# Optimization experiments

Measured on AMD Instinct MI355X. Metric: run time of the kernel, lower is better.

## Reference

```python
import jax, jax.numpy as jnp
import numpy as np

N_NODES = 50000
N_EDGES = 800000
D = 128


def gcn_conv(x, W, b, src, dst, num_nodes):
    """PyG GCNConv: x @ W, add self-loops, symmetric normalization, scatter-add, + bias."""
    x = x @ W  # [N, out]
    loop = jnp.arange(num_nodes, dtype=src.dtype)
    s = jnp.concatenate([src, loop])  # [E+N]
    d = jnp.concatenate([dst, loop])
    w = jnp.ones(s.shape[0], x.dtype)  # edge_weight=None -> ones (self-loop fill=1)
    deg = jax.ops.segment_sum(w, d, num_segments=num_nodes)  # [N]
    dinv = jnp.where(deg > 0, jax.lax.rsqrt(deg), 0.0)
    norm = dinv[s] * dinv[d]  # [E+N]
    out = jax.ops.segment_sum(x[s] * norm[:, None], d, num_segments=num_nodes)
    return out + b


def setup_inputs() -> dict:
    key = jax.random.key(0)
    ks = jax.random.split(key, 8)
    sc = 1.0 / np.sqrt(D)
    x = jax.random.normal(ks[0], (N_NODES, D), dtype=jnp.float32)
    edge_index = jax.random.randint(ks[1], (2, N_EDGES), 0, N_NODES)
    W1 = jax.random.normal(ks[2], (D, D), dtype=jnp.float32) * sc
    W2 = jax.random.normal(ks[3], (D, D), dtype=jnp.float32) * sc
    W3 = jax.random.normal(ks[4], (D, D), dtype=jnp.float32) * sc
    b1 = jnp.zeros((D,), jnp.float32)
    b2 = jnp.zeros((D,), jnp.float32)
    b3 = jnp.zeros((D,), jnp.float32)
    return {"x": x, "edge_index": edge_index, "W1": W1, "b1": b1,
            "W2": W2, "b2": b2, "W3": W3, "b3": b3}


def reference(x, edge_index, W1, b1, W2, b2, W3, b3):
    src, dst = edge_index[0], edge_index[1]
    n = x.shape[0]
    x = jax.nn.relu(gcn_conv(x, W1, b1, src, dst, n))
    x = jax.nn.relu(gcn_conv(x, W2, b2, src, dst, n))
    return gcn_conv(x, W3, b3, src, dst, n)
```

## Files before the change

kernel.cpp:

```cpp
#include <hip/hip_runtime.h>
#include <hip/hip_fp16.h>
#include <math.h>

#define D 128
#define PADH 136

typedef __attribute__((ext_vector_type(8))) _Float16 half8;
typedef __attribute__((ext_vector_type(4))) _Float16 half4v;
typedef __attribute__((ext_vector_type(4))) float f32x4;


__global__ void prep_kernel(const float* __restrict__ W1, const float* __restrict__ W2,
                            const float* __restrict__ W3, __half* __restrict__ WhT,
                            int* __restrict__ cnt, int N) {
    int i = blockIdx.x * blockDim.x + threadIdx.x;
    if (i < 3 * D * D) {
        int l = i >> 14;
        int j = i & 16383;
        int n = j >> 7, k = j & 127;
        const float* W = (l == 0) ? W1 : (l == 1) ? W2 : W3;
        WhT[(size_t)i] = __float2half(W[(size_t)k * D + n]);
    }
    if (i < N) cnt[i] = 0;
}


__global__ void count_rank_kernel(const int* __restrict__ dst, int* __restrict__ cnt,
                                  int* __restrict__ rank, int E) {
    int e0 = (blockIdx.x * blockDim.x + threadIdx.x) * 8;
    if (e0 + 7 < E) {
        int4 da = *(const int4*)(dst + e0);
        int4 db = *(const int4*)(dst + e0 + 4);
        int4 ra, rb;
        ra.x = atomicAdd(&cnt[da.x], 1);
        ra.y = atomicAdd(&cnt[da.y], 1);
        ra.z = atomicAdd(&cnt[da.z], 1);
        ra.w = atomicAdd(&cnt[da.w], 1);
        rb.x = atomicAdd(&cnt[db.x], 1);
        rb.y = atomicAdd(&cnt[db.y], 1);
        rb.z = atomicAdd(&cnt[db.z], 1);
        rb.w = atomicAdd(&cnt[db.w], 1);
        *(int4*)(rank + e0)     = ra;
        *(int4*)(rank + e0 + 4) = rb;
    } else {
        for (int e = e0; e < E; ++e) rank[e] = atomicAdd(&cnt[dst[e]], 1);
    }
}

__global__ __launch_bounds__(1024) void scan_kernel(const int* __restrict__ cnt,
                                                    int* __restrict__ rowptr,
                                                    float* __restrict__ dinv,
                                                    int N) {
    __shared__ int wsum[16];
    int tid  = threadIdx.x;
    int lane = tid & 63;
    int wid  = tid >> 6;
    int C = ((N + 4095) / 4096) * 4;
    int start = tid * C;
    int end   = start + C; if (end > N) end = N;

    int local = 0;
    int i = start;
    for (; i + 3 < end; i += 4) {
        int4 v = *(const int4*)(cnt + i);
        local += v.x + v.y + v.z + v.w;
    }
    for (; i < end; ++i) local += cnt[i];

    int sc = local;
    #pragma unroll
    for (int off = 1; off < 64; off <<= 1) {
        int t = __shfl_up(sc, off, 64);
        if (lane >= off) sc += t;
    }
    if (lane == 63) wsum[wid] = sc;
    __syncthreads();
    if (tid < 16) {
        int w = wsum[tid];
        #pragma unroll
        for (int off = 1; off < 16; off <<= 1) {
            int t = __shfl_up(w, off, 16);
            if (tid >= off) w += t;
        }
        wsum[tid] = w;
    }
    __syncthreads();
    int run = ((wid > 0) ? wsum[wid - 1] : 0) + (sc - local);

    i = start;
    for (; i + 3 < end; i += 4) {
        int4 v = *(const int4*)(cnt + i);
        int4 rp;
        rp.x = run;
        rp.y = rp.x + v.x;
        rp.z = rp.y + v.y;
        rp.w = rp.z + v.z;
        run  = rp.w + v.w;
        *(int4*)(rowptr + i) = rp;
        float4 dv;
        dv.x = rsqrtf((float)v.x + 1.0f);
        dv.y = rsqrtf((float)v.y + 1.0f);
        dv.z = rsqrtf((float)v.z + 1.0f);
        dv.w = rsqrtf((float)v.w + 1.0f);
        *(float4*)(dinv + i) = dv;
    }
    for (; i < end; ++i) {
        int v = cnt[i];
        rowptr[i] = run; run += v;
        dinv[i] = rsqrtf((float)v + 1.0f);
    }
    if (tid == 0) rowptr[N] = wsum[15];
}


__device__ __forceinline__ float4 gather2(const __half* __restrict__ g,
                                          const int* __restrict__ rowptr,
                                          const int* __restrict__ col,
                                          int r0, int r1, int lane) {
    int half = lane >> 5;
    int l32  = lane & 31;
    int hb   = half << 5;
    int row  = half ? r1 : r0;
    int s = rowptr[row], e = rowptr[row + 1];

    half4v hs = ((const half4v*)(g + (size_t)row * D))[l32];
    float4 A = make_float4((float)hs[0], (float)hs[1], (float)hs[2], (float)hs[3]);
    float4 B = make_float4(0.f, 0.f, 0.f, 0.f);

    for (int base = s; base < e; base += 32) {
        int idx = base + l32;
        int myc = (idx < e) ? col[idx] : 0;
        int nb  = min(32, e - base);
        int j = 0;
        for (; j + 8 <= nb; j += 8) {
            int c0 = __shfl(myc, hb + j + 0), c1 = __shfl(myc, hb + j + 1);
            int c2 = __shfl(myc, hb + j + 2), c3 = __shfl(myc, hb + j + 3);
            int c4 = __shfl(myc, hb + j + 4), c5 = __shfl(myc, hb + j + 5);
            int c6 = __shfl(myc, hb + j + 6), c7 = __shfl(myc, hb + j + 7);
            half4v v0 = ((const half4v*)(g + (size_t)c0 * D))[l32];
            half4v v1 = ((const half4v*)(g + (size_t)c1 * D))[l32];
            half4v v2 = ((const half4v*)(g + (size_t)c2 * D))[l32];
            half4v v3 = ((const half4v*)(g + (size_t)c3 * D))[l32];
            half4v v4 = ((const half4v*)(g + (size_t)c4 * D))[l32];
            half4v v5 = ((const half4v*)(g + (size_t)c5 * D))[l32];
            half4v v6 = ((const half4v*)(g + (size_t)c6 * D))[l32];
            half4v v7 = ((const half4v*)(g + (size_t)c7 * D))[l32];
            A.x += (float)v0[0]; A.y += (float)v0[1]; A.z += (float)v0[2]; A.w += (float)v0[3];
            B.x += (float)v1[0]; B.y += (float)v1[1]; B.z += (float)v1[2]; B.w += (float)v1[3];
            A.x += (float)v2[0]; A.y += (float)v2[1]; A.z += (float)v2[2]; A.w += (float)v2[3];
            B.x += (float)v3[0]; B.y += (float)v3[1]; B.z += (float)v3[2]; B.w += (float)v3[3];
            A.x += (float)v4[0]; A.y += (float)v4[1]; A.z += (float)v4[2]; A.w += (float)v4[3];
            B.x += (float)v5[0]; B.y += (float)v5[1]; B.z += (float)v5[2]; B.w += (float)v5[3];
            A.x += (float)v6[0]; A.y += (float)v6[1]; A.z += (float)v6[2]; A.w += (float)v6[3];
            B.x += (float)v7[0]; B.y += (float)v7[1]; B.z += (float)v7[2]; B.w += (float)v7[3];
        }
        for (; j + 4 <= nb; j += 4) {
            int c0 = __shfl(myc, hb + j + 0), c1 = __shfl(myc, hb + j + 1);
            int c2 = __shfl(myc, hb + j + 2), c3 = __shfl(myc, hb + j + 3);
            half4v v0 = ((const half4v*)(g + (size_t)c0 * D))[l32];
            half4v v1 = ((const half4v*)(g + (size_t)c1 * D))[l32];
            half4v v2 = ((const half4v*)(g + (size_t)c2 * D))[l32];
            half4v v3 = ((const half4v*)(g + (size_t)c3 * D))[l32];
            A.x += (float)v0[0]; A.y += (float)v0[1]; A.z += (float)v0[2]; A.w += (float)v0[3];
            B.x += (float)v1[0]; B.y += (float)v1[1]; B.z += (float)v1[2]; B.w += (float)v1[3];
            A.x += (float)v2[0]; A.y += (float)v2[1]; A.z += (float)v2[2]; A.w += (float)v2[3];
            B.x += (float)v3[0]; B.y += (float)v3[1]; B.z += (float)v3[2]; B.w += (float)v3[3];
        }
        for (; j < nb; ++j) {
            int c = __shfl(myc, hb + j);
            half4v v = ((const half4v*)(g + (size_t)c * D))[l32];
            A.x += (float)v[0]; A.y += (float)v[1]; A.z += (float)v[2]; A.w += (float)v[3];
        }
    }
    A.x += B.x; A.y += B.y; A.z += B.z; A.w += B.w;
    return A;
}


__global__ __launch_bounds__(256) void fill_gemm1_kernel(
    const int* __restrict__ src, const int* __restrict__ dst,
    const int* __restrict__ rank, const int* __restrict__ rowptr,
    int* __restrict__ col, int E, int fill_blocks,
    const float* __restrict__ X, const __half* __restrict__ WhT,
    const float* __restrict__ dinv, __half* __restrict__ Y, int M) {
    int tid = threadIdx.x;
    if ((int)blockIdx.x < fill_blocks) {
        int e0 = (blockIdx.x * 256 + tid) * 8;
        if (e0 + 7 < E) {
            int4 da = *(const int4*)(dst + e0);
            int4 db = *(const int4*)(dst + e0 + 4);
            int4 ra = *(const int4*)(rank + e0);
            int4 rb = *(const int4*)(rank + e0 + 4);
            int4 sa = *(const int4*)(src + e0);
            int4 sb = *(const int4*)(src + e0 + 4);
            int p0 = rowptr[da.x] + ra.x;
            int p1 = rowptr[da.y] + ra.y;
            int p2 = rowptr[da.z] + ra.z;
            int p3 = rowptr[da.w] + ra.w;
            int p4 = rowptr[db.x] + rb.x;
            int p5 = rowptr[db.y] + rb.y;
            int p6 = rowptr[db.z] + rb.z;
            int p7 = rowptr[db.w] + rb.w;
            col[p0] = sa.x; col[p1] = sa.y; col[p2] = sa.z; col[p3] = sa.w;
            col[p4] = sb.x; col[p5] = sb.y; col[p6] = sb.z; col[p7] = sb.w;
        } else {
            for (int e = e0; e < E; ++e) col[rowptr[dst[e]] + rank[e]] = src[e];
        }
        return;
    }
    int bid  = blockIdx.x - fill_blocks;
    int wave = tid >> 6;
    int lane = tid & 63;
    int quad = lane >> 4;
    int l16  = lane & 15;
    int m0   = bid * 64 + wave * 16;
    if (m0 >= M) return;

    f32x4 acc[8];
    #pragma unroll
    for (int t = 0; t < 8; ++t) acc[t] = (f32x4)0.0f;

    const float* xrow = X + (size_t)(m0 + l16) * D;

    #pragma unroll
    for (int ks = 0; ks < 4; ++ks) {
        int k0 = ks * 32 + quad * 8;
        float4 x0 = *(const float4*)(xrow + k0);
        float4 x1 = *(const float4*)(xrow + k0 + 4);
        half8 a;
        a[0] = (_Float16)x0.x; a[1] = (_Float16)x0.y;
        a[2] = (_Float16)x0.z; a[3] = (_Float16)x0.w;
        a[4] = (_Float16)x1.x; a[5] = (_Float16)x1.y;
        a[6] = (_Float16)x1.z; a[7] = (_Float16)x1.w;
        #pragma unroll
        for (int t = 0; t < 8; ++t) {
            half8 b = *(const half8*)(WhT + (size_t)(t * 16 + l16) * D + k0);
            acc[t] = __builtin_amdgcn_mfma_f32_16x16x32_f16(a, b, acc[t], 0, 0, 0);
        }
    }

    float4 dv = *(const float4*)(dinv + m0 + quad * 4);
    float dvs[4] = {dv.x, dv.y, dv.z, dv.w};
    #pragma unroll
    for (int t = 0; t < 8; ++t) {
        #pragma unroll
        for (int r = 0; r < 4; ++r) {
            int grow = m0 + quad * 4 + r;
            Y[(size_t)grow * D + t * 16 + l16] = __float2half(acc[t][r] * dvs[r]);
        }
    }
}


__global__ __launch_bounds__(256) void agg_gemm_kernel(
    const __half* __restrict__ ysIn, const int* __restrict__ rowptr,
    const int* __restrict__ col, const float* __restrict__ dinv,
    const float* __restrict__ bias, const __half* __restrict__ WhT,
    __half* __restrict__ ysOut, int M) {
    __shared__ __half lds_h[16 * PADH];
    int tid  = threadIdx.x;
    int wave = tid >> 6;
    int lane = tid & 63;
    int half = lane >> 5;
    int l32  = lane & 31;
    int rbase = blockIdx.x * 16;

    float4 bb = ((const float4*)bias)[l32];
    #pragma unroll
    for (int t = 0; t < 2; ++t) {
        int lr0 = wave * 4 + t * 2;
        int row0 = rbase + lr0;
        int row1 = row0 + 1;
        int c0 = min(row0, M - 1);
        int c1 = min(row1, M - 1);
        float4 a = gather2(ysIn, rowptr, col, c0, c1, lane);
        int myrow = half ? c1 : c0;
        float dv = dinv[myrow];
        half4v hv;
        hv[0] = (_Float16)fmaxf(bb.x + dv * a.x, 0.f);
        hv[1] = (_Float16)fmaxf(bb.y + dv * a.y, 0.f);
        hv[2] = (_Float16)fmaxf(bb.z + dv * a.z, 0.f);
        hv[3] = (_Float16)fmaxf(bb.w + dv * a.w, 0.f);
        ((half4v*)(lds_h + (size_t)(lr0 + half) * PADH))[l32] = hv;
    }
    __syncthreads();

    if (rbase >= M) return;
    int quad = lane >> 4;
    int l16  = lane & 15;
    int t0   = wave * 2;

    f32x4 acc0 = (f32x4)0.0f, acc1 = (f32x4)0.0f;
    const __half* arow = lds_h + (size_t)l16 * PADH;

    #pragma unroll
    for (int ks = 0; ks < 4; ++ks) {
        int k0 = ks * 32 + quad * 8;
        half8 a  = *(const half8*)(arow + k0);
        half8 b0 = *(const half8*)(WhT + (size_t)((t0 + 0) * 16 + l16) * D + k0);
        half8 b1 = *(const half8*)(WhT + (size_t)((t0 + 1) * 16 + l16) * D + k0);
        acc0 = __builtin_amdgcn_mfma_f32_16x16x32_f16(a, b0, acc0, 0, 0, 0);
        acc1 = __builtin_amdgcn_mfma_f32_16x16x32_f16(a, b1, acc1, 0, 0, 0);
    }

    #pragma unroll
    for (int r = 0; r < 4; ++r) {
        int grow = rbase + quad * 4 + r;
        if (grow < M) {
            float dvr = dinv[grow];
            ysOut[(size_t)grow * D + (t0 + 0) * 16 + l16] = __float2half(acc0[r] * dvr);
            ysOut[(size_t)grow * D + (t0 + 1) * 16 + l16] = __float2half(acc1[r] * dvr);
        }
    }
}


__global__ __launch_bounds__(256) void agg_final_kernel(
    const __half* __restrict__ ys, const int* __restrict__ rowptr,
    const int* __restrict__ col, const float* __restrict__ dinv,
    const float* __restrict__ b, float* __restrict__ out, int N) {
    int gwave = (blockIdx.x * blockDim.x + threadIdx.x) >> 6;
    int lane  = threadIdx.x & 63;
    int half  = lane >> 5;
    int l32   = lane & 31;
    int row0  = gwave * 2;
    if (row0 >= N) return;
    int row1  = row0 + 1;
    int c1    = min(row1, N - 1);

    float4 a = gather2(ys, rowptr, col, row0, c1, lane);
    int myrow = half ? c1 : row0;
    int orow  = row0 + half;
    if (orow < N) {
        float dv  = dinv[myrow];
        float4 bb = ((const float4*)b)[l32];
        float4 r;
        r.x = bb.x + dv * a.x;
        r.y = bb.y + dv * a.y;
        r.z = bb.z + dv * a.z;
        r.w = bb.w + dv * a.w;
        ((float4*)(out + (size_t)orow * D))[l32] = r;
    }
}


extern "C" void kernel_launch(void* const* d_in, const int* in_sizes, int n_in,
                              void* d_out, int out_size, void* d_ws, size_t ws_size,
                              hipStream_t stream) {
    const float* x   = (const float*)d_in[0];
    const int*   ei  = (const int*)d_in[1];
    const float* W1  = (const float*)d_in[2];
    const float* b1  = (const float*)d_in[3];
    const float* W2  = (const float*)d_in[4];
    const float* b2  = (const float*)d_in[5];
    const float* W3  = (const float*)d_in[6];
    const float* b3  = (const float*)d_in[7];
    float* out = (float*)d_out;

    const int N = in_sizes[0] / D;
    const int E = in_sizes[1] / 2;
    const int* src = ei;
    const int* dst = ei + E;

    char* ws = (char*)d_ws;
    size_t off = 0;
    auto alloc = [&](size_t bytes) {
        void* p = ws + off;
        off = (off + bytes + 255) & ~(size_t)255;
        return p;
    };
    __half* ys    = (__half*)alloc((size_t)N * D * sizeof(__half));
    __half* hs    = (__half*)alloc((size_t)N * D * sizeof(__half));
    int*   cnt    = (int*)alloc((size_t)N * sizeof(int));
    int*   rowptr = (int*)alloc((size_t)(N + 1) * sizeof(int));
    float* dinv   = (float*)alloc((size_t)N * sizeof(float));
    int*   rank   = (int*)alloc((size_t)E * sizeof(int));
    int*   col    = (int*)alloc((size_t)E * sizeof(int));
    __half* WhT   = (__half*)alloc((size_t)3 * D * D * sizeof(__half));
    (void)ws_size; (void)n_in; (void)out_size;

    int prep_threads = (3 * D * D > N) ? 3 * D * D : N;
    prep_kernel<<<(prep_threads + 255) / 256, 256, 0, stream>>>(W1, W2, W3, WhT, cnt, N);

    const int egrid = ((E + 7) / 8 + 255) / 256;
    count_rank_kernel<<<egrid, 256, 0, stream>>>(dst, cnt, rank, E);
    scan_kernel<<<1, 1024, 0, stream>>>(cnt, rowptr, dinv, N);

    const int gemm1_grid = (N + 63) / 64;
    fill_gemm1_kernel<<<egrid + gemm1_grid, 256, 0, stream>>>(
        src, dst, rank, rowptr, col, E, egrid, x, WhT, dinv, ys, N);

    const int agg_gemm_grid = (N + 15) / 16;
    agg_gemm_kernel<<<agg_gemm_grid, 256, 0, stream>>>(ys, rowptr, col, dinv, b1, WhT + 16384, hs, N);
    agg_gemm_kernel<<<agg_gemm_grid, 256, 0, stream>>>(hs, rowptr, col, dinv, b2, WhT + 32768, ys, N);

    const int aggf_grid = ((N + 1) / 2 * 64 + 255) / 256;
    agg_final_kernel<<<aggf_grid, 256, 0, stream>>>(ys, rowptr, col, dinv, b3, out, N);
}
```

Baseline: 294.2 us.

## Fuse all GCN stages into one cooperative persistent kernel with grid syncs

Replaces the seven-kernel launch sequence with a single cooperative mega-kernel of 1024 blocks that runs every stage (weight transpose, degree count, scan, CSR fill plus first GEMM, two agg+GEMM layers, final aggregation) separated by grid.sync. The single-block scan is replaced by a multi-block scan using per-block partials, and each block serially sums the partials of all earlier blocks. The aim is to remove launch gaps and the serial one-block scan. In exchange, the persistent grid may have lower per-stage occupancy and grid barriers add cost. If the cooperative launch fails, the code falls back to the old kernels.

```diff
diff --git a/kernel.cpp b/kernel.cpp
--- a/kernel.cpp
+++ b/kernel.cpp
@@ -1,116 +1,18 @@
 #include <hip/hip_runtime.h>
 #include <hip/hip_fp16.h>
+#include <hip/hip_cooperative_groups.h>
 #include <math.h>
 
 #define D 128
 #define PADH 136
+#define NB 1024
+#define NT 256
+
+namespace cg = cooperative_groups;
 
 typedef __attribute__((ext_vector_type(8))) _Float16 half8;
 typedef __attribute__((ext_vector_type(4))) _Float16 half4v;
 typedef __attribute__((ext_vector_type(4))) float f32x4;
-
-
-__global__ void prep_kernel(const float* __restrict__ W1, const float* __restrict__ W2,
-                            const float* __restrict__ W3, __half* __restrict__ WhT,
-                            int* __restrict__ cnt, int N) {
-    int i = blockIdx.x * blockDim.x + threadIdx.x;
-    if (i < 3 * D * D) {
-        int l = i >> 14;
-        int j = i & 16383;
-        int n = j >> 7, k = j & 127;
-        const float* W = (l == 0) ? W1 : (l == 1) ? W2 : W3;
-        WhT[(size_t)i] = __float2half(W[(size_t)k * D + n]);
-    }
-    if (i < N) cnt[i] = 0;
-}
-
-
-__global__ void count_rank_kernel(const int* __restrict__ dst, int* __restrict__ cnt,
-                                  int* __restrict__ rank, int E) {
-    int e0 = (blockIdx.x * blockDim.x + threadIdx.x) * 8;
-    if (e0 + 7 < E) {
-        int4 da = *(const int4*)(dst + e0);
-        int4 db = *(const int4*)(dst + e0 + 4);
-        int4 ra, rb;
-        ra.x = atomicAdd(&cnt[da.x], 1);
-        ra.y = atomicAdd(&cnt[da.y], 1);
-        ra.z = atomicAdd(&cnt[da.z], 1);
-        ra.w = atomicAdd(&cnt[da.w], 1);
-        rb.x = atomicAdd(&cnt[db.x], 1);
-        rb.y = atomicAdd(&cnt[db.y], 1);
-        rb.z = atomicAdd(&cnt[db.z], 1);
-        rb.w = atomicAdd(&cnt[db.w], 1);
-        *(int4*)(rank + e0)     = ra;
-        *(int4*)(rank + e0 + 4) = rb;
-    } else {
-        for (int e = e0; e < E; ++e) rank[e] = atomicAdd(&cnt[dst[e]], 1);
-    }
-}
-
-__global__ __launch_bounds__(1024) void scan_kernel(const int* __restrict__ cnt,
-                                                    int* __restrict__ rowptr,
-                                                    float* __restrict__ dinv,
-                                                    int N) {
-    __shared__ int wsum[16];
-    int tid  = threadIdx.x;
-    int lane = tid & 63;
-    int wid  = tid >> 6;
-    int C = ((N + 4095) / 4096) * 4;
-    int start = tid * C;
-    int end   = start + C; if (end > N) end = N;
-
-    int local = 0;
-    int i = start;
-    for (; i + 3 < end; i += 4) {
-        int4 v = *(const int4*)(cnt + i);
-        local += v.x + v.y + v.z + v.w;
-    }
-    for (; i < end; ++i) local += cnt[i];
-
-    int sc = local;
-    #pragma unroll
-    for (int off = 1; off < 64; off <<= 1) {
-        int t = __shfl_up(sc, off, 64);
-        if (lane >= off) sc += t;
-    }
-    if (lane == 63) wsum[wid] = sc;
-    __syncthreads();
-    if (tid < 16) {
-        int w = wsum[tid];
-        #pragma unroll
-        for (int off = 1; off < 16; off <<= 1) {
-            int t = __shfl_up(w, off, 16);
-            if (tid >= off) w += t;
-        }
-        wsum[tid] = w;
-    }
-    __syncthreads();
-    int run = ((wid > 0) ? wsum[wid - 1] : 0) + (sc - local);
-
-    i = start;
-    for (; i + 3 < end; i += 4) {
-        int4 v = *(const int4*)(cnt + i);
-        int4 rp;
-        rp.x = run;
-        rp.y = rp.x + v.x;
-        rp.z = rp.y + v.y;
-        rp.w = rp.z + v.z;
-        run  = rp.w + v.w;
-        *(int4*)(rowptr + i) = rp;
-        float4 dv;
-        dv.x = rsqrtf((float)v.x + 1.0f);
-        dv.y = rsqrtf((float)v.y + 1.0f);
-        dv.z = rsqrtf((float)v.z + 1.0f);
-        dv.w = rsqrtf((float)v.w + 1.0f);
-        *(float4*)(dinv + i) = dv;
-    }
-    for (; i < end; ++i) {
-        int v = cnt[i];
-        rowptr[i] = run; run += v;
-        dinv[i] = rsqrtf((float)v + 1.0f);
-    }
-    if (tid == 0) rowptr[N] = wsum[15];
-}
 
 
 __device__ __forceinline__ float4 gather2(const __half* __restrict__ g,
@@ -177,6 +79,359 @@
 }
 
 
+__global__ __launch_bounds__(NT, 4) void mega_kernel(
+    const float* __restrict__ X, const int* __restrict__ src, const int* __restrict__ dst,
+    const float* __restrict__ W1, const float* __restrict__ b1,
+    const float* __restrict__ W2, const float* __restrict__ b2,
+    const float* __restrict__ W3, const float* __restrict__ b3,
+    float* __restrict__ out,
+    __half* __restrict__ ys, __half* __restrict__ hs,
+    int* __restrict__ cnt, int* __restrict__ rowptr, float* __restrict__ dinv,
+    int* __restrict__ rank, int* __restrict__ col, int* __restrict__ partials,
+    __half* __restrict__ WhT, int N, int E)
+{
+    cg::grid_group grid = cg::this_grid();
+    const int tid  = threadIdx.x;
+    const int bid  = blockIdx.x;
+    const int nb   = gridDim.x;
+    const int gid  = bid * NT + tid;
+    const int gsz  = nb * NT;
+    const int lane = tid & 63;
+    const int wid  = tid >> 6;
+
+    __shared__ __half lds_h[16 * PADH];
+    __shared__ int sred[4];
+
+    for (int i = gid; i < 3 * D * D; i += gsz) {
+        int l = i >> 14, j = i & 16383, n = j >> 7, k = j & 127;
+        const float* W = (l == 0) ? W1 : (l == 1) ? W2 : W3;
+        WhT[i] = __float2half(W[(size_t)k * D + n]);
+    }
+    for (int i = gid; i < N; i += gsz) cnt[i] = 0;
+    grid.sync();
+
+    const int NO = (E + 7) / 8;
+    for (int c = gid; c < NO; c += gsz) {
+        int e0 = c * 8;
+        if (e0 + 7 < E) {
+            int4 da = *(const int4*)(dst + e0);
+            int4 db = *(const int4*)(dst + e0 + 4);
+            int4 ra, rb;
+            ra.x = atomicAdd(&cnt[da.x], 1);
+            ra.y = atomicAdd(&cnt[da.y], 1);
+            ra.z = atomicAdd(&cnt[da.z], 1);
+            ra.w = atomicAdd(&cnt[da.w], 1);
+            rb.x = atomicAdd(&cnt[db.x], 1);
+            rb.y = atomicAdd(&cnt[db.y], 1);
+            rb.z = atomicAdd(&cnt[db.z], 1);
+            rb.w = atomicAdd(&cnt[db.w], 1);
+            *(int4*)(rank + e0)     = ra;
+            *(int4*)(rank + e0 + 4) = rb;
+        } else {
+            for (int e = e0; e < E; ++e) rank[e] = atomicAdd(&cnt[dst[e]], 1);
+        }
+    }
+    grid.sync();
+
+    int4 myv = make_int4(0, 0, 0, 0);
+    int mysum = 0;
+    const int t4 = gid * 4;
+    if (t4 < N) {
+        if (t4 + 3 < N) myv = *(const int4*)(cnt + t4);
+        else {
+            myv.x = cnt[t4];
+            if (t4 + 1 < N) myv.y = cnt[t4 + 1];
+            if (t4 + 2 < N) myv.z = cnt[t4 + 2];
+        }
+        mysum = myv.x + myv.y + myv.z + myv.w;
+        dinv[t4] = rsqrtf((float)myv.x + 1.0f);
+        if (t4 + 1 < N) dinv[t4 + 1] = rsqrtf((float)myv.y + 1.0f);
+        if (t4 + 2 < N) dinv[t4 + 2] = rsqrtf((float)myv.z + 1.0f);
+        if (t4 + 3 < N) dinv[t4 + 3] = rsqrtf((float)myv.w + 1.0f);
+    }
+    {
+        int rs = mysum;
+        #pragma unroll
+        for (int off = 32; off > 0; off >>= 1) rs += __shfl_down(rs, off, 64);
+        if (lane == 0) sred[wid] = rs;
+        __syncthreads();
+        if (tid == 0) partials[bid] = sred[0] + sred[1] + sred[2] + sred[3];
+    }
+    grid.sync();
+
+    {
+        int sc = mysum;
+        #pragma unroll
+        for (int off = 1; off < 64; off <<= 1) {
+            int t = __shfl_up(sc, off, 64);
+            if (lane >= off) sc += t;
+        }
+        __syncthreads();
+        if (lane == 63) sred[wid] = sc;
+        __syncthreads();
+        int waveoff = 0;
+        #pragma unroll
+        for (int w = 0; w < 4; ++w) if (w < wid) waveoff += sred[w];
+        if (t4 < N) {
+            int base = 0;
+            for (int b = 0; b < bid; ++b) base += partials[b];
+            int run = base + waveoff + (sc - mysum);
+            rowptr[t4] = run;                 run += myv.x;
+            if (t4 + 1 < N) rowptr[t4 + 1] = run; run += myv.y;
+            if (t4 + 2 < N) rowptr[t4 + 2] = run; run += myv.z;
+            if (t4 + 3 < N) rowptr[t4 + 3] = run;
+        }
+        if (gid == 0) rowptr[N] = E;
+    }
+    grid.sync();
+
+    const int FB = nb / 2;
+    if (bid < FB) {
+        const int fsz = FB * NT;
+        for (int c = bid * NT + tid; c < NO; c += fsz) {
+            int e0 = c * 8;
+            if (e0 + 7 < E) {
+                int4 da = *(const int4*)(dst + e0);
+                int4 db = *(const int4*)(dst + e0 + 4);
+                int4 ra = *(const int4*)(rank + e0);
+                int4 rb = *(const int4*)(rank + e0 + 4);
+                int4 sa = *(const int4*)(src + e0);
+                int4 sb = *(const int4*)(src + e0 + 4);
+                col[rowptr[da.x] + ra.x] = sa.x;
+                col[rowptr[da.y] + ra.y] = sa.y;
+                col[rowptr[da.z] + ra.z] = sa.z;
+                col[rowptr[da.w] + ra.w] = sa.w;
+                col[rowptr[db.x] + rb.x] = sb.x;
+                col[rowptr[db.y] + rb.y] = sb.y;
+                col[rowptr[db.z] + rb.z] = sb.z;
+                col[rowptr[db.w] + rb.w] = sb.w;
+            } else {
+                for (int e = e0; e < E; ++e) col[rowptr[dst[e]] + rank[e]] = src[e];
+            }
+        }
+    } else {
+        const int ntile = (N + 63) / 64;
+        const int quad = lane >> 4, l16 = lane & 15;
+        for (int t = bid - FB; t < ntile; t += nb - FB) {
+            int m0 = t * 64 + wid * 16;
+            if (m0 < N) {
+                f32x4 acc[8];
+                #pragma unroll
+                for (int q = 0; q < 8; ++q) acc[q] = (f32x4)0.0f;
+                const float* xrow = X + (size_t)(m0 + l16) * D;
+                #pragma unroll
+                for (int ks = 0; ks < 4; ++ks) {
+                    int k0 = ks * 32 + quad * 8;
+                    float4 x0 = *(const float4*)(xrow + k0);
+                    float4 x1 = *(const float4*)(xrow + k0 + 4);
+                    half8 a;
+                    a[0] = (_Float16)x0.x; a[1] = (_Float16)x0.y;
+                    a[2] = (_Float16)x0.z; a[3] = (_Float16)x0.w;
+                    a[4] = (_Float16)x1.x; a[5] = (_Float16)x1.y;
+                    a[6] = (_Float16)x1.z; a[7] = (_Float16)x1.w;
+                    #pragma unroll
+                    for (int q = 0; q < 8; ++q) {
+                        half8 b = *(const half8*)(WhT + (size_t)(q * 16 + l16) * D + k0);
+                        acc[q] = __builtin_amdgcn_mfma_f32_16x16x32_f16(a, b, acc[q], 0, 0, 0);
+                    }
+                }
+                float4 dv = *(const float4*)(dinv + m0 + quad * 4);
+                float dvs[4] = {dv.x, dv.y, dv.z, dv.w};
+                #pragma unroll
+                for (int q = 0; q < 8; ++q) {
+                    #pragma unroll
+                    for (int r = 0; r < 4; ++r) {
+                        int grow = m0 + quad * 4 + r;
+                        ys[(size_t)grow * D + q * 16 + l16] = __float2half(acc[q][r] * dvs[r]);
+                    }
+                }
+            }
+        }
+    }
+    grid.sync();
+
+    #pragma unroll 1
+    for (int layer = 0; layer < 2; ++layer) {
+        const __half* gin   = (layer == 0) ? ys : hs;
+        __half*       gout  = (layer == 0) ? hs : ys;
+        const float*  bias  = (layer == 0) ? b1 : b2;
+        const __half* WhTl  = WhT + (layer == 0 ? 16384 : 32768);
+
+        const int hf  = lane >> 5;
+        const int l32 = lane & 31;
+        const int quad = lane >> 4, l16 = lane & 15;
+        const int t0 = wid * 2;
+        float4 bb = ((const float4*)bias)[l32];
+        const int ntile = (N + 15) / 16;
+
+        for (int tile = bid; tile < ntile; tile += nb) {
+            int rbase = tile * 16;
+            #pragma unroll
+            for (int t = 0; t < 2; ++t) {
+                int lr0 = wid * 4 + t * 2;
+                int row0 = rbase + lr0;
+                int c0 = min(row0, N - 1);
+                int c1 = min(row0 + 1, N - 1);
+                float4 a = gather2(gin, rowptr, col, c0, c1, lane);
+                int myrow = hf ? c1 : c0;
+                float dv = dinv[myrow];
+                half4v hv;
+                hv[0] = (_Float16)fmaxf(bb.x + dv * a.x, 0.f);
+                hv[1] = (_Float16)fmaxf(bb.y + dv * a.y, 0.f);
+                hv[2] = (_Float16)fmaxf(bb.z + dv * a.z, 0.f);
+                hv[3] = (_Float16)fmaxf(bb.w + dv * a.w, 0.f);
+                ((half4v*)(lds_h + (size_t)(lr0 + hf) * PADH))[l32] = hv;
+            }
+            __syncthreads();
+
+            f32x4 acc0 = (f32x4)0.0f, acc1 = (f32x4)0.0f;
+            const __half* arow = lds_h + (size_t)l16 * PADH;
+            #pragma unroll
+            for (int ks = 0; ks < 4; ++ks) {
+                int k0 = ks * 32 + quad * 8;
+                half8 a  = *(const half8*)(arow + k0);
+                half8 b0 = *(const half8*)(WhTl + (size_t)((t0 + 0) * 16 + l16) * D + k0);
+                half8 b1v = *(const half8*)(WhTl + (size_t)((t0 + 1) * 16 + l16) * D + k0);
+                acc0 = __builtin_amdgcn_mfma_f32_16x16x32_f16(a, b0, acc0, 0, 0, 0);
+                acc1 = __builtin_amdgcn_mfma_f32_16x16x32_f16(a, b1v, acc1, 0, 0, 0);
+            }
+            #pragma unroll
+            for (int r = 0; r < 4; ++r) {
+                int grow = rbase + quad * 4 + r;
+                if (grow < N) {
+                    float dvr = dinv[grow];
+                    gout[(size_t)grow * D + (t0 + 0) * 16 + l16] = __float2half(acc0[r] * dvr);
+                    gout[(size_t)grow * D + (t0 + 1) * 16 + l16] = __float2half(acc1[r] * dvr);
+                }
+            }
+            __syncthreads();
+        }
+        grid.sync();
+    }
+
+    {
+        const int gw = gid >> 6;
+        const int nw = gsz >> 6;
+        const int hf = lane >> 5;
+        const int l32 = lane & 31;
+        const int npair = (N + 1) / 2;
+        for (int p = gw; p < npair; p += nw) {
+            int row0 = p * 2;
+            int c1 = min(row0 + 1, N - 1);
+            float4 a = gather2(ys, rowptr, col, row0, c1, lane);
+            int myrow = hf ? c1 : row0;
+            int orow = row0 + hf;
+            if (orow < N) {
+                float dv  = dinv[myrow];
+                float4 bb = ((const float4*)b3)[l32];
+                float4 r;
+                r.x = bb.x + dv * a.x;
+                r.y = bb.y + dv * a.y;
+                r.z = bb.z + dv * a.z;
+                r.w = bb.w + dv * a.w;
+                ((float4*)(out + (size_t)orow * D))[l32] = r;
+            }
+        }
+    }
+}
+
+
+__global__ void prep_kernel(const float* __restrict__ W1, const float* __restrict__ W2,
+                            const float* __restrict__ W3, __half* __restrict__ WhT,
+                            int* __restrict__ cnt, int N) {
+    int i = blockIdx.x * blockDim.x + threadIdx.x;
+    if (i < 3 * D * D) {
+        int l = i >> 14, j = i & 16383, n = j >> 7, k = j & 127;
+        const float* W = (l == 0) ? W1 : (l == 1) ? W2 : W3;
+        WhT[(size_t)i] = __float2half(W[(size_t)k * D + n]);
+    }
+    if (i < N) cnt[i] = 0;
+}
+
+__global__ void count_rank_kernel(const int* __restrict__ dst, int* __restrict__ cnt,
+                                  int* __restrict__ rank, int E) {
+    int e0 = (blockIdx.x * blockDim.x + threadIdx.x) * 8;
+    if (e0 + 7 < E) {
+        int4 da = *(const int4*)(dst + e0);
+        int4 db = *(const int4*)(dst + e0 + 4);
+        int4 ra, rb;
+        ra.x = atomicAdd(&cnt[da.x], 1);
+        ra.y = atomicAdd(&cnt[da.y], 1);
+        ra.z = atomicAdd(&cnt[da.z], 1);
+        ra.w = atomicAdd(&cnt[da.w], 1);
+        rb.x = atomicAdd(&cnt[db.x], 1);
+        rb.y = atomicAdd(&cnt[db.y], 1);
+        rb.z = atomicAdd(&cnt[db.z], 1);
+        rb.w = atomicAdd(&cnt[db.w], 1);
+        *(int4*)(rank + e0)     = ra;
+        *(int4*)(rank + e0 + 4) = rb;
+    } else {
+        for (int e = e0; e < E; ++e) rank[e] = atomicAdd(&cnt[dst[e]], 1);
+    }
+}
+
+__global__ __launch_bounds__(1024) void scan_kernel(const int* __restrict__ cnt,
+                                                    int* __restrict__ rowptr,
+                                                    float* __restrict__ dinv,
+                                                    int N) {
+    __shared__ int wsum[16];
+    int tid  = threadIdx.x;
+    int lane = tid & 63;
+    int wid  = tid >> 6;
+    int C = ((N + 4095) / 4096) * 4;
+    int start = tid * C;
+    int end   = start + C; if (end > N) end = N;
+
+    int local = 0;
+    int i = start;
+    for (; i + 3 < end; i += 4) {
+        int4 v = *(const int4*)(cnt + i);
+        local += v.x + v.y + v.z + v.w;
+    }
+    for (; i < end; ++i) local += cnt[i];
+
+    int sc = local;
+    #pragma unroll
+    for (int off = 1; off < 64; off <<= 1) {
+        int t = __shfl_up(sc, off, 64);
+        if (lane >= off) sc += t;
+    }
+    if (lane == 63) wsum[wid] = sc;
+    __syncthreads();
+    if (tid < 16) {
+        int w = wsum[tid];
+        #pragma unroll
+        for (int off = 1; off < 16; off <<= 1) {
+            int t = __shfl_up(w, off, 16);
+            if (tid >= off) w += t;
+        }
+        wsum[tid] = w;
+    }
+    __syncthreads();
+    int run = ((wid > 0) ? wsum[wid - 1] : 0) + (sc - local);
+
+    i = start;
+    for (; i + 3 < end; i += 4) {
+        int4 v = *(const int4*)(cnt + i);
+        int4 rp;
+        rp.x = run; rp.y = rp.x + v.x; rp.z = rp.y + v.y; rp.w = rp.z + v.z;
+        run = rp.w + v.w;
+        *(int4*)(rowptr + i) = rp;
+        float4 dv;
+        dv.x = rsqrtf((float)v.x + 1.0f);
+        dv.y = rsqrtf((float)v.y + 1.0f);
+        dv.z = rsqrtf((float)v.z + 1.0f);
+        dv.w = rsqrtf((float)v.w + 1.0f);
+        *(float4*)(dinv + i) = dv;
+    }
+    for (; i < end; ++i) {
+        int v = cnt[i];
+        rowptr[i] = run; run += v;
+        dinv[i] = rsqrtf((float)v + 1.0f);
+    }
+    if (tid == 0) rowptr[N] = wsum[15];
+}
+
 __global__ __launch_bounds__(256) void fill_gemm1_kernel(
     const int* __restrict__ src, const int* __restrict__ dst,
     const int* __restrict__ rank, const int* __restrict__ rowptr,
@@ -193,16 +448,14 @@
             int4 rb = *(const int4*)(rank + e0 + 4);
             int4 sa = *(const int4*)(src + e0);
             int4 sb = *(const int4*)(src + e0 + 4);
-            int p0 = rowptr[da.x] + ra.x;
-            int p1 = rowptr[da.y] + ra.y;
-            int p2 = rowptr[da.z] + ra.z;
-            int p3 = rowptr[da.w] + ra.w;
-            int p4 = rowptr[db.x] + rb.x;
-            int p5 = rowptr[db.y] + rb.y;
-            int p6 = rowptr[db.z] + rb.z;
-            int p7 = rowptr[db.w] + rb.w;
-            col[p0] = sa.x; col[p1] = sa.y; col[p2] = sa.z; col[p3] = sa.w;
-            col[p4] = sb.x; col[p5] = sb.y; col[p6] = sb.z; col[p7] = sb.w;
+            col[rowptr[da.x] + ra.x] = sa.x;
+            col[rowptr[da.y] + ra.y] = sa.y;
+            col[rowptr[da.z] + ra.z] = sa.z;
+            col[rowptr[da.w] + ra.w] = sa.w;
+            col[rowptr[db.x] + rb.x] = sb.x;
+            col[rowptr[db.y] + rb.y] = sb.y;
+            col[rowptr[db.z] + rb.z] = sb.z;
+            col[rowptr[db.w] + rb.w] = sb.w;
         } else {
             for (int e = e0; e < E; ++e) col[rowptr[dst[e]] + rank[e]] = src[e];
         }
@@ -219,9 +472,7 @@
     f32x4 acc[8];
     #pragma unroll
     for (int t = 0; t < 8; ++t) acc[t] = (f32x4)0.0f;
-
     const float* xrow = X + (size_t)(m0 + l16) * D;
-
     #pragma unroll
     for (int ks = 0; ks < 4; ++ks) {
         int k0 = ks * 32 + quad * 8;
@@ -238,7 +489,6 @@
             acc[t] = __builtin_amdgcn_mfma_f32_16x16x32_f16(a, b, acc[t], 0, 0, 0);
         }
     }
-
     float4 dv = *(const float4*)(dinv + m0 + quad * 4);
     float dvs[4] = {dv.x, dv.y, dv.z, dv.w};
     #pragma unroll
@@ -250,7 +500,6 @@
         }
     }
 }
-
 
 __global__ __launch_bounds__(256) void agg_gemm_kernel(
     const __half* __restrict__ ysIn, const int* __restrict__ rowptr,
@@ -261,7 +510,7 @@
     int tid  = threadIdx.x;
     int wave = tid >> 6;
     int lane = tid & 63;
-    int half = lane >> 5;
+    int hf   = lane >> 5;
     int l32  = lane & 31;
     int rbase = blockIdx.x * 16;
 
@@ -270,18 +519,17 @@
     for (int t = 0; t < 2; ++t) {
         int lr0 = wave * 4 + t * 2;
         int row0 = rbase + lr0;
-        int row1 = row0 + 1;
         int c0 = min(row0, M - 1);
-        int c1 = min(row1, M - 1);
+        int c1 = min(row0 + 1, M - 1);
         float4 a = gather2(ysIn, rowptr, col, c0, c1, lane);
-        int myrow = half ? c1 : c0;
+        int myrow = hf ? c1 : c0;
         float dv = dinv[myrow];
         half4v hv;
         hv[0] = (_Float16)fmaxf(bb.x + dv * a.x, 0.f);
         hv[1] = (_Float16)fmaxf(bb.y + dv * a.y, 0.f);
         hv[2] = (_Float16)fmaxf(bb.z + dv * a.z, 0.f);
         hv[3] = (_Float16)fmaxf(bb.w + dv * a.w, 0.f);
-        ((half4v*)(lds_h + (size_t)(lr0 + half) * PADH))[l32] = hv;
+        ((half4v*)(lds_h + (size_t)(lr0 + hf) * PADH))[l32] = hv;
     }
     __syncthreads();
 
@@ -292,7 +540,6 @@
 
     f32x4 acc0 = (f32x4)0.0f, acc1 = (f32x4)0.0f;
     const __half* arow = lds_h + (size_t)l16 * PADH;
-
     #pragma unroll
     for (int ks = 0; ks < 4; ++ks) {
         int k0 = ks * 32 + quad * 8;
@@ -302,7 +549,6 @@
         acc0 = __builtin_amdgcn_mfma_f32_16x16x32_f16(a, b0, acc0, 0, 0, 0);
         acc1 = __builtin_amdgcn_mfma_f32_16x16x32_f16(a, b1, acc1, 0, 0, 0);
     }
-
     #pragma unroll
     for (int r = 0; r < 4; ++r) {
         int grow = rbase + quad * 4 + r;
@@ -314,23 +560,21 @@
     }
 }
 
-
 __global__ __launch_bounds__(256) void agg_final_kernel(
     const __half* __restrict__ ys, const int* __restrict__ rowptr,
     const int* __restrict__ col, const float* __restrict__ dinv,
     const float* __restrict__ b, float* __restrict__ out, int N) {
     int gwave = (blockIdx.x * blockDim.x + threadIdx.x) >> 6;
     int lane  = threadIdx.x & 63;
-    int half  = lane >> 5;
+    int hf    = lane >> 5;
     int l32   = lane & 31;
     int row0  = gwave * 2;
     if (row0 >= N) return;
-    int row1  = row0 + 1;
-    int c1    = min(row1, N - 1);
+    int c1 = min(row0 + 1, N - 1);
 
     float4 a = gather2(ys, rowptr, col, row0, c1, lane);
-    int myrow = half ? c1 : row0;
-    int orow  = row0 + half;
+    int myrow = hf ? c1 : row0;
+    int orow  = row0 + hf;
     if (orow < N) {
         float dv  = dinv[myrow];
         float4 bb = ((const float4*)b)[l32];
@@ -357,8 +601,8 @@
     const float* b3  = (const float*)d_in[7];
     float* out = (float*)d_out;
 
-    const int N = in_sizes[0] / D;
-    const int E = in_sizes[1] / 2;
+    int N = in_sizes[0] / D;
+    int E = in_sizes[1] / 2;
     const int* src = ei;
     const int* dst = ei + E;
 
@@ -376,24 +620,28 @@
     float* dinv   = (float*)alloc((size_t)N * sizeof(float));
     int*   rank   = (int*)alloc((size_t)E * sizeof(int));
     int*   col    = (int*)alloc((size_t)E * sizeof(int));
+    int*   partials = (int*)alloc((size_t)NB * sizeof(int));
     __half* WhT   = (__half*)alloc((size_t)3 * D * D * sizeof(__half));
     (void)ws_size; (void)n_in; (void)out_size;
 
-    int prep_threads = (3 * D * D > N) ? 3 * D * D : N;
-    prep_kernel<<<(prep_threads + 255) / 256, 256, 0, stream>>>(W1, W2, W3, WhT, cnt, N);
-
-    const int egrid = ((E + 7) / 8 + 255) / 256;
-    count_rank_kernel<<<egrid, 256, 0, stream>>>(dst, cnt, rank, E);
-    scan_kernel<<<1, 1024, 0, stream>>>(cnt, rowptr, dinv, N);
-
-    const int gemm1_grid = (N + 63) / 64;
-    fill_gemm1_kernel<<<egrid + gemm1_grid, 256, 0, stream>>>(
-        src, dst, rank, rowptr, col, E, egrid, x, WhT, dinv, ys, N);
-
-    const int agg_gemm_grid = (N + 15) / 16;
-    agg_gemm_kernel<<<agg_gemm_grid, 256, 0, stream>>>(ys, rowptr, col, dinv, b1, WhT + 16384, hs, N);
-    agg_gemm_kernel<<<agg_gemm_grid, 256, 0, stream>>>(hs, rowptr, col, dinv, b2, WhT + 32768, ys, N);
-
-    const int aggf_grid = ((N + 1) / 2 * 64 + 255) / 256;
-    agg_final_kernel<<<aggf_grid, 256, 0, stream>>>(ys, rowptr, col, dinv, b3, out, N);
-}
+    void* args[] = { &x, &src, &dst, &W1, &b1, &W2, &b2, &W3, &b3, &out,
+                     &ys, &hs, &cnt, &rowptr, &dinv, &rank, &col, &partials,
+                     &WhT, &N, &E };
+    hipError_t err = hipLaunchCooperativeKernel((const void*)mega_kernel,
+                                                dim3(NB), dim3(NT), args, 0, stream);
+    if (err != hipSuccess) {
+        int prep_threads = (3 * D * D > N) ? 3 * D * D : N;
+        prep_kernel<<<(prep_threads + 255) / 256, 256, 0, stream>>>(W1, W2, W3, WhT, cnt, N);
+        const int egrid = ((E + 7) / 8 + 255) / 256;
+        count_rank_kernel<<<egrid, 256, 0, stream>>>(dst, cnt, rank, E);
+        scan_kernel<<<1, 1024, 0, stream>>>(cnt, rowptr, dinv, N);
+        const int gemm1_grid = (N + 63) / 64;
+        fill_gemm1_kernel<<<egrid + gemm1_grid, 256, 0, stream>>>(
+            src, dst, rank, rowptr, col, E, egrid, x, WhT, dinv, ys, N);
+        const int agg_gemm_grid = (N + 15) / 16;
+        agg_gemm_kernel<<<agg_gemm_grid, 256, 0, stream>>>(ys, rowptr, col, dinv, b1, WhT + 16384, hs, N);
+        agg_gemm_kernel<<<agg_gemm_grid, 256, 0, stream>>>(hs, rowptr, col, dinv, b2, WhT + 32768, ys, N);
+        const int aggf_grid = ((N + 1) / 2 * 64 + 255) / 256;
+        agg_final_kernel<<<aggf_grid, 256, 0, stream>>>(ys, rowptr, col, dinv, b3, out, N);
+    }
+}
```

Result: slower. 1.068 ms (+263.1%).
